# Kernel tuning notes

Hardware: AMD Instinct MI355X
Metric: run time of the kernel (lower is better)

Reference implementation:

```python
import jax, jax.numpy as jnp
import numpy as np

EPS = 1e-08
STRIDE = 1
KSIZE = 3

def setup_inputs() -> dict:
    key = jax.random.key(0)
    k1, k2, k3 = jax.random.split(key, 3)
    b, cin, cout, hw = 8, 512, 512, 64
    img = jax.random.normal(k1, (b, cin, hw, hw), dtype=jnp.float32)
    s = jax.random.normal(k2, (b, cin), dtype=jnp.float32)
    # xavier_normal init scale: sqrt(2/(fan_in+fan_out)), fan = c*k*k
    fan = cin * KSIZE * KSIZE
    std = np.sqrt(2.0 / (fan + cout * KSIZE * KSIZE)).astype(np.float32)
    weight = jax.random.normal(k3, (cout, cin, KSIZE, KSIZE), dtype=jnp.float32) * std
    return {"img": img, "s": s, "weight": weight}

def _modulated_weights(weight, s):
    # weight: [O,I,k,k], s: [B,I] -> [B,O,I,k,k]
    w = weight[None] * (s[:, None, :, None, None] + 1.0)
    d = jax.lax.rsqrt(jnp.sum(w * w, axis=(2, 3, 4), keepdims=True) + EPS)
    return w * d

def _conv_one(x, w, padding):
    # x: [I,H,W], w: [O,I,k,k] -> [O,H',W']
    out = jax.lax.conv_general_dilated(
        x[None], w, window_strides=(STRIDE, STRIDE),
        padding=((padding, padding), (padding, padding)),
        dimension_numbers=("NCHW", "OIHW", "NCHW"))
    return out[0]

def reference(img, s, weight):
    b, c, h, wdt = img.shape
    assert h == wdt
    padding = ((STRIDE - 1) * h - STRIDE + KSIZE) // 2
    ws = _modulated_weights(weight, s)           # [B,O,I,k,k]
    out = jax.vmap(lambda x, w: _conv_one(x, w, padding))(img, ws)
    return out
```

## Files before the change

kernel.cpp:

```cpp
#include <hip/hip_runtime.h>

typedef __attribute__((ext_vector_type(8))) short bf16x8;
typedef __attribute__((ext_vector_type(4))) float f32x4;
typedef __attribute__((ext_vector_type(8))) unsigned short u16x8;
typedef unsigned int u32;
typedef unsigned short u16;

#define CIN 512
#define CO  512
#define HH  64
#define WW  64
#define BB  8
#define HP  66
#define WPAD 68
#define HPW (HP*WPAD)
#define KK  4608

#define SIG_BYTES  (BB*CO*4)
#define WMOD_ELEMS ((size_t)BB*9*64*CO*8)
#define WMOD_BYTES (WMOD_ELEMS*2)
#define IMGT_ELEMS ((size_t)BB*64*HP*WPAD*8)
#define IMGT_BYTES (IMGT_ELEMS*2)
#define WS_NEED    ((size_t)SIG_BYTES + WMOD_BYTES + IMGT_BYTES)

__device__ __forceinline__ u16 f2bf(float f) {
  union { float f; u32 u; } v; v.f = f;
  u32 r = (v.u + 0x7FFFu + ((v.u >> 16) & 1u)) >> 16;
  return (u16)r;
}

__global__ void k_sigma(const float* __restrict__ weight, const float* __restrict__ s,
                        float* __restrict__ sigma) {
  int o = blockIdx.x;
  int tid = threadIdx.x;
  const float* wrow = weight + (size_t)o * KK;
  float acc[BB];
#pragma unroll
  for (int b = 0; b < BB; ++b) acc[b] = 0.f;
  for (int e = tid; e < KK; e += 256) {
    float w = wrow[e];
    float w2 = w * w;
    int i = e / 9;
#pragma unroll
    for (int b = 0; b < BB; ++b) {
      float m = s[b * CIN + i] + 1.0f;
      acc[b] += w2 * m * m;
    }
  }
#pragma unroll
  for (int b = 0; b < BB; ++b) {
#pragma unroll
    for (int off = 32; off >= 1; off >>= 1)
      acc[b] += __shfl_down(acc[b], off);
  }
  __shared__ float red[4][BB];
  int wv = tid >> 6, ln = tid & 63;
  if (ln == 0) {
#pragma unroll
    for (int b = 0; b < BB; ++b) red[wv][b] = acc[b];
  }
  __syncthreads();
  if (tid < BB) {
    float t = red[0][tid] + red[1][tid] + red[2][tid] + red[3][tid];
    sigma[tid * CO + o] = rsqrtf(t + 1e-8f);
  }
}

__global__ __launch_bounds__(256) void k_wmod(const float* __restrict__ weight,
                                              const float* __restrict__ s,
                                              const float* __restrict__ sigma,
                                              u16* __restrict__ wmod) {
  __shared__ float lw[16][577];
  int bid = blockIdx.x;
  int oc = bid & 31, ic = bid >> 5;
  int o0 = oc * 16;
  int tid = threadIdx.x;
  const float* wsrc = weight + (size_t)o0 * KK + ic * 576;
#pragma unroll
  for (int k = 0; k < 9; ++k) {
    int f4 = tid + k * 256;
    int row = f4 / 144;
    int col = f4 - row * 144;
    float4 v = *(const float4*)(wsrc + (size_t)row * KK + col * 4);
    lw[row][col*4+0]=v.x; lw[row][col*4+1]=v.y; lw[row][col*4+2]=v.z; lw[row][col*4+3]=v.w;
  }
  __syncthreads();
  int o_l = tid & 15, kg_l = (tid >> 4) & 7;
#pragma unroll
  for (int k = 0; k < 36; ++k) {
    int bt = k * 2 + (tid >> 7);
    int b = bt / 9;
    int t = bt - b * 9;
    int o = o0 + o_l;
    float sig = sigma[b * CO + o];
    u16x8 ov;
#pragma unroll
    for (int j = 0; j < 8; ++j) {
      int il = kg_l * 8 + j;
      float w = lw[o_l][il * 9 + t];
      float m = s[b * CIN + ic * 64 + il] + 1.0f;
      ov[j] = f2bf(w * m * sig);
    }
    *(u16x8*)(wmod + ((size_t)(bt * 64 + (ic * 8 + kg_l)) * CO + o) * 8) = ov;
  }
}

__global__ void k_pad(u16* __restrict__ imgt) {
  int gid = blockIdx.x * 256 + threadIdx.x;
  int grp = gid & 63;
  int pos = gid >> 6;
  int b = pos / 264;
  int pr = pos - b * 264;
  int yp, xp;
  if (pr < 136) { yp = (pr < 68) ? 0 : 65; xp = (pr < 68) ? pr : pr - 68; }
  else { int q = pr - 136; yp = 1 + (q >> 1); xp = (q & 1) ? 67 : 0; }
  u16x8 z = {0,0,0,0,0,0,0,0};
  *(u16x8*)(imgt + (((size_t)(b * 64 + grp) * HP + yp) * WPAD + xp) * 8) = z;
}

__global__ void k_imgt(const float* __restrict__ img, u16* __restrict__ imgt) {
  int bid = blockIdx.x;
  int ic = bid & 7;  int r = bid >> 3;
  int xc = r & 1;    r >>= 1;
  int y  = r & 63;   int b = r >> 6;
  int tid = threadIdx.x;
  __shared__ float lt[64][33];
  {
    int ii = tid >> 2, xq = tid & 3;
    const float* src = img + (((size_t)(b * CIN + ic * 64 + ii)) * HH + y) * WW + xc * 32 + xq * 8;
    float4 v0 = *(const float4*)src;
    float4 v1 = *(const float4*)(src + 4);
    int xb = xq * 8;
    lt[ii][xb+0]=v0.x; lt[ii][xb+1]=v0.y; lt[ii][xb+2]=v0.z; lt[ii][xb+3]=v0.w;
    lt[ii][xb+4]=v1.x; lt[ii][xb+5]=v1.y; lt[ii][xb+6]=v1.z; lt[ii][xb+7]=v1.w;
  }
  __syncthreads();
  int xl = tid >> 3, iq = tid & 7;
  u16x8 ov;
#pragma unroll
  for (int j = 0; j < 8; ++j) ov[j] = f2bf(lt[iq*8+j][xl]);
  size_t dst = (((size_t)(b * 64 + ic * 8 + iq) * HP + (y + 1)) * WPAD + (xc * 32 + xl + 1)) * 8;
  *(u16x8*)(imgt + dst) = ov;
}

__device__ __forceinline__ void async16(const u16* g, void* lds) {
  __builtin_amdgcn_global_load_lds((const __attribute__((address_space(1))) u32*)g,
                                   (__attribute__((address_space(3))) u32*)lds, 16, 0, 0);
}

__global__ __launch_bounds__(512, 2) void k_conv(const u16* __restrict__ wmod,
                                                 const u16* __restrict__ imgt,
                                                 float* __restrict__ out) {
  __shared__ alignas(16) u16 abuf[2][3][8192];
  int bid0 = blockIdx.x;
  int bid  = (bid0 & 7) * 32 + (bid0 >> 3);
  int b  = bid >> 5;
  int ot = (bid >> 4) & 1;
  int pt = bid & 15;
  int y0 = pt * 4, obase = ot * 256;
  int tid = threadIdx.x;
  int wave = tid >> 6, lane = tid & 63;
  int wm = wave >> 2, wn = wave & 3;
  int col0 = lane & 15, kg = lane >> 4;

  const u16* awsrc0 = wmod + (((size_t)(b * 576 + (tid >> 8))) * 512 + obase + (tid & 255)) * 8;
  const u16* awsrc1 = awsrc0 + 2 * 512 * 8;

  const u16* pB = imgt + (((size_t)(b * 64 + kg) * HP + (y0 + wn)) * WPAD + col0) * 8;

  f32x4 zero = {0.f, 0.f, 0.f, 0.f};
  f32x4 acc[8][4];
#pragma unroll
  for (int i = 0; i < 8; ++i)
#pragma unroll
    for (int j = 0; j < 4; ++j) acc[i][j] = zero;

  bf16x8 bregE[4], bregO[4];

#define STAGE3(slot, iccv, rv) do { \
  _Pragma("unroll") \
  for (int c_ = 0; c_ < 3; ++c_) { \
    int aoff_ = ((3 * (rv) + c_) * 64 + (iccv) * 4) * 4096; \
    async16(awsrc0 + aoff_, (void*)(&abuf[slot][c_][0] + (size_t)tid * 8)); \
    async16(awsrc1 + aoff_, (void*)(&abuf[slot][c_][0] + (size_t)(tid + 512) * 8)); \
  } } while (0)

#define BPF(dst, iccv, tv) do { \
  const u16* pb_ = pB + (size_t)(iccv) * (4 * HPW * 8); \
  dst[0] = *(const bf16x8*)(pb_ + (((tv)/3) * WPAD +  0 + ((tv)%3)) * 8); \
  dst[1] = *(const bf16x8*)(pb_ + (((tv)/3) * WPAD + 16 + ((tv)%3)) * 8); \
  dst[2] = *(const bf16x8*)(pb_ + (((tv)/3) * WPAD + 32 + ((tv)%3)) * 8); \
  dst[3] = *(const bf16x8*)(pb_ + (((tv)/3) * WPAD + 48 + ((tv)%3)) * 8); \
} while (0)

#define COMPUTE(slot, c_, BR) do { \
  const u16* ab_ = &abuf[slot][c_][(kg * 256 + wm * 128 + col0) * 8]; \
  bf16x8 a_[8]; \
  _Pragma("unroll") \
  for (int am = 0; am < 8; ++am) a_[am] = *(const bf16x8*)(ab_ + am * 128); \
  __builtin_amdgcn_s_setprio(1); \
  _Pragma("unroll") \
  for (int am = 0; am < 8; ++am) { \
    acc[am][0] = __builtin_amdgcn_mfma_f32_16x16x32_bf16(a_[am], BR[0], acc[am][0], 0, 0, 0); \
    acc[am][1] = __builtin_amdgcn_mfma_f32_16x16x32_bf16(a_[am], BR[1], acc[am][1], 0, 0, 0); \
    acc[am][2] = __builtin_amdgcn_mfma_f32_16x16x32_bf16(a_[am], BR[2], acc[am][2], 0, 0, 0); \
    acc[am][3] = __builtin_amdgcn_mfma_f32_16x16x32_bf16(a_[am], BR[3], acc[am][3], 0, 0, 0); \
  } \
  __builtin_amdgcn_s_setprio(0); \
} while (0)

#define GROUP(g, B0, B1) do { \
  if (ii < 7 || (g) < 5) STAGE3((((g) + 1) & 1), ii2 + ((g) + 1) / 3, ((g) + 1) % 3); \
  BPF(B1, ii2 + (3 * (g) + 1) / 9, (3 * (g) + 1) % 9); \
  COMPUTE(((g) & 1), 0, B0); \
  BPF(B0, ii2 + (3 * (g) + 2) / 9, (3 * (g) + 2) % 9); \
  COMPUTE(((g) & 1), 1, B1); \
  if (ii < 7 || 3 * (g) + 3 < 18) BPF(B1, ii2 + (3 * (g) + 3) / 9, (3 * (g) + 3) % 9); \
  COMPUTE(((g) & 1), 2, B0); \
  asm volatile("s_waitcnt vmcnt(12)" ::: "memory"); \
  __builtin_amdgcn_s_barrier(); \
  __builtin_amdgcn_sched_barrier(0); \
} while (0)

  {
    const int ii2 = 0;
    STAGE3(0, 0, 0);
    BPF(bregE, 0, 0);
  }
  asm volatile("s_waitcnt vmcnt(4)" ::: "memory");
  __builtin_amdgcn_s_barrier();
  __builtin_amdgcn_sched_barrier(0);

  for (int ii = 0; ii < 8; ++ii) {
    const int ii2 = 2 * ii;
    GROUP(0, bregE, bregO);
    GROUP(1, bregO, bregE);
    GROUP(2, bregE, bregO);
    GROUP(3, bregO, bregE);
    GROUP(4, bregE, bregO);
    GROUP(5, bregO, bregE);
  }
#undef GROUP
#undef COMPUTE
#undef BPF
#undef STAGE3

  int y = y0 + wn;
#pragma unroll
  for (int am = 0; am < 8; ++am) {
    int o = obase + wm * 128 + am * 16 + kg * 4;
#pragma unroll
    for (int an = 0; an < 4; ++an) {
      int x = an * 16 + col0;
      float* op = out + (((size_t)(b * CO + o)) * HH + y) * WW + x;
#pragma unroll
      for (int rg = 0; rg < 4; ++rg)
        op[(size_t)rg * HH * WW] = acc[am][an][rg];
    }
  }
}

__global__ void k_naive(const float* __restrict__ img, const float* __restrict__ s,
                        const float* __restrict__ weight, const float* __restrict__ sigma,
                        float* __restrict__ out) {
  int bid = blockIdx.x;
  int y = bid & 63; int r = bid >> 6; int o = r & 511; int b = r >> 9;
  int x = threadIdx.x;
  float sig = sigma[b * CO + o];
  float acc = 0.f;
  for (int i = 0; i < CIN; ++i) {
    float m = s[b * CIN + i] + 1.0f;
    const float* wp = weight + ((size_t)o * CIN + i) * 9;
    const float* ip = img + ((size_t)(b * CIN + i)) * HH * WW;
#pragma unroll
    for (int ky = 0; ky < 3; ++ky) {
      int yy = y + ky - 1;
      if (yy < 0 || yy > 63) continue;
#pragma unroll
      for (int kx = 0; kx < 3; ++kx) {
        int xx = x + kx - 1;
        float iv = (xx >= 0 && xx < 64) ? ip[yy * 64 + xx] : 0.f;
        acc += wp[ky * 3 + kx] * m * iv;
      }
    }
  }
  out[((size_t)(b * CO + o) * HH + y) * WW + x] = acc * sig;
}

extern "C" void kernel_launch(void* const* d_in, const int* in_sizes, int n_in,
                              void* d_out, int out_size, void* d_ws, size_t ws_size,
                              hipStream_t stream) {
  const float* img    = (const float*)d_in[0];
  const float* s      = (const float*)d_in[1];
  const float* weight = (const float*)d_in[2];
  float* out = (float*)d_out;
  char* ws = (char*)d_ws;
  float* sigma = (float*)ws;

  if (ws_size >= WS_NEED) {
    u16* wmod = (u16*)(ws + SIG_BYTES);
    u16* imgt = (u16*)(ws + SIG_BYTES + WMOD_BYTES);
    k_sigma<<<512, 256, 0, stream>>>(weight, s, sigma);
    k_wmod<<<256, 256, 0, stream>>>(weight, s, sigma, wmod);
    k_pad<<<528, 256, 0, stream>>>(imgt);
    k_imgt<<<8192, 256, 0, stream>>>(img, imgt);
    k_conv<<<256, 512, 0, stream>>>(wmod, imgt, out);
  } else {
    k_sigma<<<512, 256, 0, stream>>>(weight, s, sigma);
    k_naive<<<BB * CO * HH, 64, 0, stream>>>(img, s, weight, sigma, out);
  }
}
```

Baseline: 171.0 us.

## Shrink conv tile to 128x128 with 256-thread blocks and 1024-block grid

Changes the implicit-GEMM conv block tile from 256 output channels by 4 rows to 128 channels by 2 rows. Blocks drop to 256 threads and the grid grows from 256 to 1024 blocks, so the 256 CUs of MI355X get more blocks each and occupancy rises. The K pipeline is restructured from groups of three taps to a rolling loop that stages two taps per step with double-buffered LDS and a rotating tap/channel index. The cost is less operand reuse per block, so weights and image rows are loaded more times overall, plus more barriers per unit of work.

```diff
diff --git a/kernel.cpp b/kernel.cpp
--- a/kernel.cpp
+++ b/kernel.cpp
@@ -148,59 +148,60 @@
                                    (__attribute__((address_space(3))) u32*)lds, 16, 0, 0);
 }
 
-__global__ __launch_bounds__(512, 2) void k_conv(const u16* __restrict__ wmod,
+__global__ __launch_bounds__(256, 4) void k_conv(const u16* __restrict__ wmod,
                                                  const u16* __restrict__ imgt,
                                                  float* __restrict__ out) {
-  __shared__ alignas(16) u16 abuf[2][3][8192];
+  __shared__ alignas(16) u16 abuf[2][2][4096];
   int bid0 = blockIdx.x;
-  int bid  = (bid0 & 7) * 32 + (bid0 >> 3);
-  int b  = bid >> 5;
-  int ot = (bid >> 4) & 1;
-  int pt = bid & 15;
-  int y0 = pt * 4, obase = ot * 256;
+  int bid  = (bid0 & 7) * 128 + (bid0 >> 3);
+  int b  = bid >> 7;
+  int rem = bid & 127;
+  int ot = rem >> 5;
+  int pt = rem & 31;
+  int y0 = pt * 2, obase = ot * 128;
   int tid = threadIdx.x;
   int wave = tid >> 6, lane = tid & 63;
-  int wm = wave >> 2, wn = wave & 3;
+  int wm = wave >> 1, wn = wave & 1;
   int col0 = lane & 15, kg = lane >> 4;
 
-  const u16* awsrc0 = wmod + (((size_t)(b * 576 + (tid >> 8))) * 512 + obase + (tid & 255)) * 8;
+  const u16* awsrc0 = wmod + (((size_t)(b * 576 + (tid >> 7))) * 512 + obase + (tid & 127)) * 8;
   const u16* awsrc1 = awsrc0 + 2 * 512 * 8;
 
   const u16* pB = imgt + (((size_t)(b * 64 + kg) * HP + (y0 + wn)) * WPAD + col0) * 8;
 
   f32x4 zero = {0.f, 0.f, 0.f, 0.f};
-  f32x4 acc[8][4];
-#pragma unroll
-  for (int i = 0; i < 8; ++i)
+  f32x4 acc[4][4];
+#pragma unroll
+  for (int i = 0; i < 4; ++i)
 #pragma unroll
     for (int j = 0; j < 4; ++j) acc[i][j] = zero;
 
-  bf16x8 bregE[4], bregO[4];
-
-#define STAGE3(slot, iccv, rv) do { \
+  bf16x8 B0[4], B1[4];
+
+#define STAGE1(slot, cc, iccv, tv) do { \
+  int aoff_ = ((tv) * 64 + (iccv) * 4) * 4096; \
+  async16(awsrc0 + aoff_, (void*)(&abuf[slot][cc][0] + (size_t)tid * 8)); \
+  async16(awsrc1 + aoff_, (void*)(&abuf[slot][cc][0] + (size_t)(tid + 256) * 8)); \
+} while (0)
+
+#define BPF(dst, iccv, tv) do { \
+  int ky_ = ((tv) >= 6) ? 2 : (((tv) >= 3) ? 1 : 0); \
+  int kx_ = (tv) - 3 * ky_; \
+  const u16* pb_ = pB + (size_t)(iccv) * (4 * HPW * 8); \
+  dst[0] = *(const bf16x8*)(pb_ + (ky_ * WPAD +  0 + kx_) * 8); \
+  dst[1] = *(const bf16x8*)(pb_ + (ky_ * WPAD + 16 + kx_) * 8); \
+  dst[2] = *(const bf16x8*)(pb_ + (ky_ * WPAD + 32 + kx_) * 8); \
+  dst[3] = *(const bf16x8*)(pb_ + (ky_ * WPAD + 48 + kx_) * 8); \
+} while (0)
+
+#define COMPUTE(slot, cc, BR) do { \
+  const u16* ab_ = &abuf[slot][cc][(kg * 128 + wm * 64 + col0) * 8]; \
+  bf16x8 a_[4]; \
   _Pragma("unroll") \
-  for (int c_ = 0; c_ < 3; ++c_) { \
-    int aoff_ = ((3 * (rv) + c_) * 64 + (iccv) * 4) * 4096; \
-    async16(awsrc0 + aoff_, (void*)(&abuf[slot][c_][0] + (size_t)tid * 8)); \
-    async16(awsrc1 + aoff_, (void*)(&abuf[slot][c_][0] + (size_t)(tid + 512) * 8)); \
-  } } while (0)
-
-#define BPF(dst, iccv, tv) do { \
-  const u16* pb_ = pB + (size_t)(iccv) * (4 * HPW * 8); \
-  dst[0] = *(const bf16x8*)(pb_ + (((tv)/3) * WPAD +  0 + ((tv)%3)) * 8); \
-  dst[1] = *(const bf16x8*)(pb_ + (((tv)/3) * WPAD + 16 + ((tv)%3)) * 8); \
-  dst[2] = *(const bf16x8*)(pb_ + (((tv)/3) * WPAD + 32 + ((tv)%3)) * 8); \
-  dst[3] = *(const bf16x8*)(pb_ + (((tv)/3) * WPAD + 48 + ((tv)%3)) * 8); \
-} while (0)
-
-#define COMPUTE(slot, c_, BR) do { \
-  const u16* ab_ = &abuf[slot][c_][(kg * 256 + wm * 128 + col0) * 8]; \
-  bf16x8 a_[8]; \
-  _Pragma("unroll") \
-  for (int am = 0; am < 8; ++am) a_[am] = *(const bf16x8*)(ab_ + am * 128); \
+  for (int am = 0; am < 4; ++am) a_[am] = *(const bf16x8*)(ab_ + am * 128); \
   __builtin_amdgcn_s_setprio(1); \
   _Pragma("unroll") \
-  for (int am = 0; am < 8; ++am) { \
+  for (int am = 0; am < 4; ++am) { \
     acc[am][0] = __builtin_amdgcn_mfma_f32_16x16x32_bf16(a_[am], BR[0], acc[am][0], 0, 0, 0); \
     acc[am][1] = __builtin_amdgcn_mfma_f32_16x16x32_bf16(a_[am], BR[1], acc[am][1], 0, 0, 0); \
     acc[am][2] = __builtin_amdgcn_mfma_f32_16x16x32_bf16(a_[am], BR[2], acc[am][2], 0, 0, 0); \
@@ -209,46 +210,40 @@
   __builtin_amdgcn_s_setprio(0); \
 } while (0)
 
-#define GROUP(g, B0, B1) do { \
-  if (ii < 7 || (g) < 5) STAGE3((((g) + 1) & 1), ii2 + ((g) + 1) / 3, ((g) + 1) % 3); \
-  BPF(B1, ii2 + (3 * (g) + 1) / 9, (3 * (g) + 1) % 9); \
-  COMPUTE(((g) & 1), 0, B0); \
-  BPF(B0, ii2 + (3 * (g) + 2) / 9, (3 * (g) + 2) % 9); \
-  COMPUTE(((g) & 1), 1, B1); \
-  if (ii < 7 || 3 * (g) + 3 < 18) BPF(B1, ii2 + (3 * (g) + 3) / 9, (3 * (g) + 3) % 9); \
-  COMPUTE(((g) & 1), 2, B0); \
-  asm volatile("s_waitcnt vmcnt(12)" ::: "memory"); \
-  __builtin_amdgcn_s_barrier(); \
-  __builtin_amdgcn_sched_barrier(0); \
-} while (0)
-
-  {
-    const int ii2 = 0;
-    STAGE3(0, 0, 0);
-    BPF(bregE, 0, 0);
-  }
+  STAGE1(0, 0, 0, 0);
+  STAGE1(0, 1, 0, 1);
+  BPF(B0, 0, 0);
   asm volatile("s_waitcnt vmcnt(4)" ::: "memory");
   __builtin_amdgcn_s_barrier();
   __builtin_amdgcn_sched_barrier(0);
 
-  for (int ii = 0; ii < 8; ++ii) {
-    const int ii2 = 2 * ii;
-    GROUP(0, bregE, bregO);
-    GROUP(1, bregO, bregE);
-    GROUP(2, bregE, bregO);
-    GROUP(3, bregO, bregE);
-    GROUP(4, bregE, bregO);
-    GROUP(5, bregO, bregE);
-  }
-#undef GROUP
+  int i0 = 0, t0 = 0;
+  for (int gg = 0; gg < 72; ++gg) {
+    int slot = gg & 1, ns = slot ^ 1;
+    int tB = t0 + 1, iB = i0; if (tB >= 9) { tB -= 9; ++iB; }
+    int tC = tB + 1, iC = iB; if (tC >= 9) { tC -= 9; ++iC; }
+    int tD = tC + 1, iD = iC; if (tD >= 9) { tD -= 9; ++iD; }
+
+    if (gg < 71) { STAGE1(ns, 0, iC, tC); STAGE1(ns, 1, iD, tD); }
+    BPF(B1, iB, tB);
+    COMPUTE(slot, 0, B0);
+    if (gg < 71) BPF(B0, iC, tC);
+    COMPUTE(slot, 1, B1);
+    if (gg < 71) {
+      asm volatile("s_waitcnt vmcnt(8)" ::: "memory");
+      __builtin_amdgcn_s_barrier();
+      __builtin_amdgcn_sched_barrier(0);
+    }
+    t0 = tC; i0 = iC;
+  }
 #undef COMPUTE
 #undef BPF
-#undef STAGE3
+#undef STAGE1
 
   int y = y0 + wn;
 #pragma unroll
-  for (int am = 0; am < 8; ++am) {
-    int o = obase + wm * 128 + am * 16 + kg * 4;
+  for (int am = 0; am < 4; ++am) {
+    int o = obase + wm * 64 + am * 16 + kg * 4;
 #pragma unroll
     for (int an = 0; an < 4; ++an) {
       int x = an * 16 + col0;
@@ -304,7 +299,7 @@
     k_wmod<<<256, 256, 0, stream>>>(weight, s, sigma, wmod);
     k_pad<<<528, 256, 0, stream>>>(imgt);
     k_imgt<<<8192, 256, 0, stream>>>(img, imgt);
-    k_conv<<<256, 512, 0, stream>>>(wmod, imgt, out);
+    k_conv<<<1024, 256, 0, stream>>>(wmod, imgt, out);
   } else {
     k_sigma<<<512, 256, 0, stream>>>(weight, s, sigma);
     k_naive<<<BB * CO * HH, 64, 0, stream>>>(img, s, weight, sigma, out);
```

After: 190.3 us. +11.3%, slower.

## Restructure conv pipeline with XOR-swizzled LDS weight tiles and 64-wide K steps

Applied to the files above, without the earlier changes.

Replaces the 3-slot weight staging with a 2-buffer layout where each stage loads a 64-channel K-slice per tap into LDS using an XOR swizzle to avoid bank conflicts on ds_read. The main loop becomes 72 steps, each issuing four async global-to-LDS loads and splitting the MFMA work into four clusters of 4x4 tiles interleaved with image-operand loads. This aims to cut LDS bank conflicts and simplify the schedule, at the cost of more barriers per K and a different register footprint.

```diff
diff --git a/kernel.cpp b/kernel.cpp
--- a/kernel.cpp
+++ b/kernel.cpp
@@ -151,7 +151,7 @@
 __global__ __launch_bounds__(512, 2) void k_conv(const u16* __restrict__ wmod,
                                                  const u16* __restrict__ imgt,
                                                  float* __restrict__ out) {
-  __shared__ alignas(16) u16 abuf[2][3][8192];
+  __shared__ alignas(16) u16 abuf[2][16384];
   int bid0 = blockIdx.x;
   int bid  = (bid0 & 7) * 32 + (bid0 >> 3);
   int b  = bid >> 5;
@@ -163,10 +163,24 @@
   int wm = wave >> 2, wn = wave & 3;
   int col0 = lane & 15, kg = lane >> 4;
 
-  const u16* awsrc0 = wmod + (((size_t)(b * 576 + (tid >> 8))) * 512 + obase + (tid & 255)) * 8;
-  const u16* awsrc1 = awsrc0 + 2 * 512 * 8;
+  const u16* asrc[4];
+  int wq[4];
+#pragma unroll
+  for (int q = 0; q < 4; ++q) {
+    int W = (tid + q * 512) * 16;
+    int L = W ^ (((W >> 7) & 7) << 4);
+    int o = L >> 7;
+    int kgl = (L >> 4) & 7;
+    wq[q] = W;
+    asrc[q] = wmod + ((size_t)(b * 576 + kgl) * 512 + obase + o) * 8;
+  }
 
   const u16* pB = imgt + (((size_t)(b * 64 + kg) * HP + (y0 + wn)) * WPAD + col0) * 8;
+
+  int arow = (wm * 128 + col0) * 128;
+  int xm   = (col0 & 7) << 4;
+  int inn0 = (kg * 16) ^ xm;
+  int inn1 = (kg * 16 + 64) ^ xm;
 
   f32x4 zero = {0.f, 0.f, 0.f, 0.f};
   f32x4 acc[8][4];
@@ -175,75 +189,73 @@
 #pragma unroll
     for (int j = 0; j < 4; ++j) acc[i][j] = zero;
 
-  bf16x8 bregE[4], bregO[4];
-
-#define STAGE3(slot, iccv, rv) do { \
+  bf16x8 BA[4], BB_[4], B1[4];
+
+#define STAGE(sn, bufsel) do { \
   _Pragma("unroll") \
-  for (int c_ = 0; c_ < 3; ++c_) { \
-    int aoff_ = ((3 * (rv) + c_) * 64 + (iccv) * 4) * 4096; \
-    async16(awsrc0 + aoff_, (void*)(&abuf[slot][c_][0] + (size_t)tid * 8)); \
-    async16(awsrc1 + aoff_, (void*)(&abuf[slot][c_][0] + (size_t)(tid + 512) * 8)); \
-  } } while (0)
-
-#define BPF(dst, iccv, tv) do { \
-  const u16* pb_ = pB + (size_t)(iccv) * (4 * HPW * 8); \
-  dst[0] = *(const bf16x8*)(pb_ + (((tv)/3) * WPAD +  0 + ((tv)%3)) * 8); \
-  dst[1] = *(const bf16x8*)(pb_ + (((tv)/3) * WPAD + 16 + ((tv)%3)) * 8); \
-  dst[2] = *(const bf16x8*)(pb_ + (((tv)/3) * WPAD + 32 + ((tv)%3)) * 8); \
-  dst[3] = *(const bf16x8*)(pb_ + (((tv)/3) * WPAD + 48 + ((tv)%3)) * 8); \
+  for (int q = 0; q < 4; ++q) \
+    async16(asrc[q] + (size_t)(sn) * 32768, (void*)((char*)&abuf[bufsel][0] + wq[q])); \
 } while (0)
 
-#define COMPUTE(slot, c_, BR) do { \
-  const u16* ab_ = &abuf[slot][c_][(kg * 256 + wm * 128 + col0) * 8]; \
-  bf16x8 a_[8]; \
-  _Pragma("unroll") \
-  for (int am = 0; am < 8; ++am) a_[am] = *(const bf16x8*)(ab_ + am * 128); \
+#define BLOAD(dst, sn, kk) do { \
+  int t_ = (sn) >> 3, ic_ = (sn) & 7; \
+  int ky_ = (t_ >= 6) ? 2 : ((t_ >= 3) ? 1 : 0); \
+  int kx_ = t_ - 3 * ky_; \
+  const u16* pb_ = pB + ((size_t)(ic_ * 8 + (kk) * 4) * HPW + ky_ * WPAD + kx_) * 8; \
+  dst[0] = *(const bf16x8*)(pb_ + 0 * 128); \
+  dst[1] = *(const bf16x8*)(pb_ + 1 * 128); \
+  dst[2] = *(const bf16x8*)(pb_ + 2 * 128); \
+  dst[3] = *(const bf16x8*)(pb_ + 3 * 128); \
+} while (0)
+
+#define CLUSTER(bufsel, h, kk, BR) do { \
+  const char* ab_ = (const char*)&abuf[bufsel][0] + arow + ((kk) ? inn1 : inn0); \
+  bf16x8 a0 = *(const bf16x8*)(ab_ + ((h) * 4 + 0) * 2048); \
+  bf16x8 a1 = *(const bf16x8*)(ab_ + ((h) * 4 + 1) * 2048); \
+  bf16x8 a2 = *(const bf16x8*)(ab_ + ((h) * 4 + 2) * 2048); \
+  bf16x8 a3 = *(const bf16x8*)(ab_ + ((h) * 4 + 3) * 2048); \
   __builtin_amdgcn_s_setprio(1); \
   _Pragma("unroll") \
-  for (int am = 0; am < 8; ++am) { \
-    acc[am][0] = __builtin_amdgcn_mfma_f32_16x16x32_bf16(a_[am], BR[0], acc[am][0], 0, 0, 0); \
-    acc[am][1] = __builtin_amdgcn_mfma_f32_16x16x32_bf16(a_[am], BR[1], acc[am][1], 0, 0, 0); \
-    acc[am][2] = __builtin_amdgcn_mfma_f32_16x16x32_bf16(a_[am], BR[2], acc[am][2], 0, 0, 0); \
-    acc[am][3] = __builtin_amdgcn_mfma_f32_16x16x32_bf16(a_[am], BR[3], acc[am][3], 0, 0, 0); \
+  for (int an = 0; an < 4; ++an) { \
+    acc[(h)*4+0][an] = __builtin_amdgcn_mfma_f32_16x16x32_bf16(a0, BR[an], acc[(h)*4+0][an], 0, 0, 0); \
+    acc[(h)*4+1][an] = __builtin_amdgcn_mfma_f32_16x16x32_bf16(a1, BR[an], acc[(h)*4+1][an], 0, 0, 0); \
+    acc[(h)*4+2][an] = __builtin_amdgcn_mfma_f32_16x16x32_bf16(a2, BR[an], acc[(h)*4+2][an], 0, 0, 0); \
+    acc[(h)*4+3][an] = __builtin_amdgcn_mfma_f32_16x16x32_bf16(a3, BR[an], acc[(h)*4+3][an], 0, 0, 0); \
   } \
   __builtin_amdgcn_s_setprio(0); \
 } while (0)
 
-#define GROUP(g, B0, B1) do { \
-  if (ii < 7 || (g) < 5) STAGE3((((g) + 1) & 1), ii2 + ((g) + 1) / 3, ((g) + 1) % 3); \
-  BPF(B1, ii2 + (3 * (g) + 1) / 9, (3 * (g) + 1) % 9); \
-  COMPUTE(((g) & 1), 0, B0); \
-  BPF(B0, ii2 + (3 * (g) + 2) / 9, (3 * (g) + 2) % 9); \
-  COMPUTE(((g) & 1), 1, B1); \
-  if (ii < 7 || 3 * (g) + 3 < 18) BPF(B1, ii2 + (3 * (g) + 3) / 9, (3 * (g) + 3) % 9); \
-  COMPUTE(((g) & 1), 2, B0); \
-  asm volatile("s_waitcnt vmcnt(12)" ::: "memory"); \
+#define STEP(s_, bufsel, BK0, BKN) do { \
+  int sn_ = ((s_) < 71) ? (s_) + 1 : 71; \
+  STAGE(sn_, (bufsel) ^ 1); \
+  __builtin_amdgcn_sched_barrier(0); \
+  BLOAD(B1, (s_), 1); \
+  CLUSTER(bufsel, 0, 0, BK0); \
+  BLOAD(BKN, sn_, 0); \
+  CLUSTER(bufsel, 1, 0, BK0); \
+  CLUSTER(bufsel, 0, 1, B1); \
+  CLUSTER(bufsel, 1, 1, B1); \
+  asm volatile("s_waitcnt vmcnt(4)" ::: "memory"); \
   __builtin_amdgcn_s_barrier(); \
   __builtin_amdgcn_sched_barrier(0); \
 } while (0)
 
-  {
-    const int ii2 = 0;
-    STAGE3(0, 0, 0);
-    BPF(bregE, 0, 0);
-  }
+  STAGE(0, 0);
+  __builtin_amdgcn_sched_barrier(0);
+  BLOAD(BA, 0, 0);
   asm volatile("s_waitcnt vmcnt(4)" ::: "memory");
   __builtin_amdgcn_s_barrier();
   __builtin_amdgcn_sched_barrier(0);
 
-  for (int ii = 0; ii < 8; ++ii) {
-    const int ii2 = 2 * ii;
-    GROUP(0, bregE, bregO);
-    GROUP(1, bregO, bregE);
-    GROUP(2, bregE, bregO);
-    GROUP(3, bregO, bregE);
-    GROUP(4, bregE, bregO);
-    GROUP(5, bregO, bregE);
-  }
-#undef GROUP
-#undef COMPUTE
-#undef BPF
-#undef STAGE3
+  for (int j = 0; j < 36; ++j) {
+    int s = 2 * j;
+    STEP(s,     0, BA,  BB_);
+    STEP(s + 1, 1, BB_, BA);
+  }
+#undef STEP
+#undef CLUSTER
+#undef BLOAD
+#undef STAGE
 
   int y = y0 + wn;
 #pragma unroll
```

After: 208.9 us. 22.1% more time.

## Switch conv MFMA from 16x16x32 to 32x32x16 bf16 tiles

Applied to the files above, without the earlier changes.

Replaces the 16x16x32 bf16 MFMA tiling with 32x32x16 instructions. This changes the per-lane mapping of A fragments from LDS, the B fragment loads from the transposed image, and the accumulator layout and output store indexing. The larger tiles need fewer A/B register loads per FLOP and use the higher-throughput-per-issue 32x32 MFMA. The risk is the altered LDS access pattern, which may cause bank conflicts, and the K split across two A halves must still match the staged layout.

```diff
diff --git a/kernel.cpp b/kernel.cpp
--- a/kernel.cpp
+++ b/kernel.cpp
@@ -2,6 +2,7 @@
 
 typedef __attribute__((ext_vector_type(8))) short bf16x8;
 typedef __attribute__((ext_vector_type(4))) float f32x4;
+typedef __attribute__((ext_vector_type(16))) float f32x16;
 typedef __attribute__((ext_vector_type(8))) unsigned short u16x8;
 typedef unsigned int u32;
 typedef unsigned short u16;
@@ -161,19 +162,22 @@
   int tid = threadIdx.x;
   int wave = tid >> 6, lane = tid & 63;
   int wm = wave >> 2, wn = wave & 3;
-  int col0 = lane & 15, kg = lane >> 4;
+  int l31 = lane & 31, lh = lane >> 5;
 
   const u16* awsrc0 = wmod + (((size_t)(b * 576 + (tid >> 8))) * 512 + obase + (tid & 255)) * 8;
   const u16* awsrc1 = awsrc0 + 2 * 512 * 8;
 
-  const u16* pB = imgt + (((size_t)(b * 64 + kg) * HP + (y0 + wn)) * WPAD + col0) * 8;
-
-  f32x4 zero = {0.f, 0.f, 0.f, 0.f};
-  f32x4 acc[8][4];
-#pragma unroll
-  for (int i = 0; i < 8; ++i)
-#pragma unroll
-    for (int j = 0; j < 4; ++j) acc[i][j] = zero;
+  const u16* pB = imgt + (((size_t)(b * 64 + lh) * HP + (y0 + wn)) * WPAD + l31) * 8;
+
+  const int abase16 = (lh * 256 + wm * 128 + l31) * 8;
+
+  f32x16 acc[4][2];
+#pragma unroll
+  for (int i = 0; i < 4; ++i)
+#pragma unroll
+    for (int j = 0; j < 2; ++j)
+#pragma unroll
+      for (int e = 0; e < 16; ++e) acc[i][j][e] = 0.f;
 
   bf16x8 bregE[4], bregO[4];
 
@@ -186,25 +190,31 @@
   } } while (0)
 
 #define BPF(dst, iccv, tv) do { \
-  const u16* pb_ = pB + (size_t)(iccv) * (4 * HPW * 8); \
-  dst[0] = *(const bf16x8*)(pb_ + (((tv)/3) * WPAD +  0 + ((tv)%3)) * 8); \
-  dst[1] = *(const bf16x8*)(pb_ + (((tv)/3) * WPAD + 16 + ((tv)%3)) * 8); \
-  dst[2] = *(const bf16x8*)(pb_ + (((tv)/3) * WPAD + 32 + ((tv)%3)) * 8); \
-  dst[3] = *(const bf16x8*)(pb_ + (((tv)/3) * WPAD + 48 + ((tv)%3)) * 8); \
+  const u16* pb_ = pB + ((size_t)((iccv) * 4) * HPW + ((tv)/3) * WPAD + ((tv)%3)) * 8; \
+  dst[0] = *(const bf16x8*)(pb_); \
+  dst[1] = *(const bf16x8*)(pb_ + 32 * 8); \
+  dst[2] = *(const bf16x8*)(pb_ + 2 * HPW * 8); \
+  dst[3] = *(const bf16x8*)(pb_ + (2 * HPW + 32) * 8); \
 } while (0)
 
 #define COMPUTE(slot, c_, BR) do { \
-  const u16* ab_ = &abuf[slot][c_][(kg * 256 + wm * 128 + col0) * 8]; \
-  bf16x8 a_[8]; \
+  const u16* ab_ = &abuf[slot][c_][abase16]; \
+  bf16x8 a0_[4], a1_[4]; \
   _Pragma("unroll") \
-  for (int am = 0; am < 8; ++am) a_[am] = *(const bf16x8*)(ab_ + am * 128); \
+  for (int rb = 0; rb < 4; ++rb) { \
+    a0_[rb] = *(const bf16x8*)(ab_ + rb * 256); \
+    a1_[rb] = *(const bf16x8*)(ab_ + rb * 256 + 4096); \
+  } \
   __builtin_amdgcn_s_setprio(1); \
   _Pragma("unroll") \
-  for (int am = 0; am < 8; ++am) { \
-    acc[am][0] = __builtin_amdgcn_mfma_f32_16x16x32_bf16(a_[am], BR[0], acc[am][0], 0, 0, 0); \
-    acc[am][1] = __builtin_amdgcn_mfma_f32_16x16x32_bf16(a_[am], BR[1], acc[am][1], 0, 0, 0); \
-    acc[am][2] = __builtin_amdgcn_mfma_f32_16x16x32_bf16(a_[am], BR[2], acc[am][2], 0, 0, 0); \
-    acc[am][3] = __builtin_amdgcn_mfma_f32_16x16x32_bf16(a_[am], BR[3], acc[am][3], 0, 0, 0); \
+  for (int rb = 0; rb < 4; ++rb) { \
+    acc[rb][0] = __builtin_amdgcn_mfma_f32_32x32x16_bf16(a0_[rb], BR[0], acc[rb][0], 0, 0, 0); \
+    acc[rb][1] = __builtin_amdgcn_mfma_f32_32x32x16_bf16(a0_[rb], BR[1], acc[rb][1], 0, 0, 0); \
+  } \
+  _Pragma("unroll") \
+  for (int rb = 0; rb < 4; ++rb) { \
+    acc[rb][0] = __builtin_amdgcn_mfma_f32_32x32x16_bf16(a1_[rb], BR[2], acc[rb][0], 0, 0, 0); \
+    acc[rb][1] = __builtin_amdgcn_mfma_f32_32x32x16_bf16(a1_[rb], BR[3], acc[rb][1], 0, 0, 0); \
   } \
   __builtin_amdgcn_s_setprio(0); \
 } while (0)
@@ -246,16 +256,17 @@
 #undef STAGE3
 
   int y = y0 + wn;
-#pragma unroll
-  for (int am = 0; am < 8; ++am) {
-    int o = obase + wm * 128 + am * 16 + kg * 4;
-#pragma unroll
-    for (int an = 0; an < 4; ++an) {
-      int x = an * 16 + col0;
-      float* op = out + (((size_t)(b * CO + o)) * HH + y) * WW + x;
-#pragma unroll
-      for (int rg = 0; rg < 4; ++rg)
-        op[(size_t)rg * HH * WW] = acc[am][an][rg];
+  int rbase = 4 * lh;
+#pragma unroll
+  for (int rb = 0; rb < 4; ++rb) {
+#pragma unroll
+    for (int cb = 0; cb < 2; ++cb) {
+      int x = cb * 32 + l31;
+#pragma unroll
+      for (int rg = 0; rg < 16; ++rg) {
+        int o = obase + wm * 128 + rb * 32 + rbase + (rg & 3) + 8 * (rg >> 2);
+        out[(((size_t)(b * CO + o)) * HH + y) * WW + x] = acc[rb][cb][rg];
+      }
     }
   }
 }
```

After: 177.8 us. 1.04x slower.
